# Kernel tuning notes

Hardware: AMD Instinct MI355X
Metric: run time of the kernel (lower is better)

The kernel has to match this reference:

```python
import jax, jax.numpy as jnp
import numpy as np

B, T, C, H = 4, 2048, 1024, 16
D = C // H  # head_dim = 64

def setup_inputs() -> dict:
    key = jax.random.key(0)
    k1, k2, k3 = jax.random.split(key, 3)
    x = jax.random.normal(k1, (B, T, C), dtype=jnp.float32)
    Wqkv = jax.random.normal(k2, (C, 3 * C), dtype=jnp.float32) * (C ** -0.5)
    Wout = jax.random.normal(k3, (C, C), dtype=jnp.float32) * (C ** -0.5)
    return {"x": x, "Wqkv": Wqkv, "Wout": Wout}

def reference(x, Wqkv, Wout):
    b, t, c = x.shape
    scale = D ** -0.5
    qkv = x @ Wqkv  # [B,T,3C]
    q, k, v = jnp.split(qkv, 3, axis=-1)
    # [B,H,T,D]
    q = q.reshape(b, t, H, D).transpose(0, 2, 1, 3)
    k = k.reshape(b, t, H, D).transpose(0, 2, 1, 3)
    v = v.reshape(b, t, H, D).transpose(0, 2, 1, 3)
    scores = jnp.einsum('bhqd,bhkd->bhqk', q, k) * scale
    causal = jnp.tril(jnp.ones((t, t), dtype=bool))
    scores = jnp.where(causal, scores, -jnp.inf)
    attn = jax.nn.softmax(scores, axis=-1)
    out = jnp.einsum('bhqk,bhkd->bhqd', attn, v)
    out = out.transpose(0, 2, 1, 3).reshape(b, t, c)
    return out @ Wout
```

## Files before the change

### kernel.cpp

```cpp
#include <hip/hip_runtime.h>
#include <hip/hip_bf16.h>

#define DEV __device__ __forceinline__

typedef __attribute__((ext_vector_type(4))) float f32x4;
typedef __attribute__((ext_vector_type(8))) __bf16 bf16x8;
typedef __attribute__((ext_vector_type(8))) unsigned short u16x8;
typedef __attribute__((ext_vector_type(4))) unsigned short u16x4;

DEV unsigned short f2b(float x) {
  unsigned int u = __builtin_bit_cast(unsigned int, x);
  unsigned int r = (u + 0x7fffu + ((u >> 16) & 1u)) >> 16;
  return (unsigned short)r;
}

DEV unsigned int cvtpk(float a, float b) {
  unsigned int r;
  asm("v_cvt_pk_bf16_f32 %0, %1, %2" : "=v"(r) : "v"(a), "v"(b));
  return r;
}

DEV f32x4 mfma16(u16x8 a, u16x8 b, f32x4 c) {
  return __builtin_amdgcn_mfma_f32_16x16x32_bf16(
      __builtin_bit_cast(bf16x8, a), __builtin_bit_cast(bf16x8, b), c, 0, 0, 0);
}

DEV void async16(const unsigned short* g, unsigned short* l) {
  __builtin_amdgcn_global_load_lds(
      (const __attribute__((address_space(1))) void*)g,
      (__attribute__((address_space(3))) void*)l, 16, 0, 0);
}


__global__ void k_convert(const float* __restrict__ in, unsigned short* __restrict__ out, int n8) {
  int i = blockIdx.x * 256 + threadIdx.x;
  if (i >= n8) return;
  const float4* p = (const float4*)in + (size_t)i * 2;
  float4 a = p[0], b = p[1];
  u16x8 v;
  v[0] = f2b(a.x); v[1] = f2b(a.y); v[2] = f2b(a.z); v[3] = f2b(a.w);
  v[4] = f2b(b.x); v[5] = f2b(b.y); v[6] = f2b(b.z); v[7] = f2b(b.w);
  *((u16x8*)out + i) = v;
}

__global__ void k_transpose(const float* __restrict__ in, unsigned short* __restrict__ out,
                            int R, int Cc) {
  __shared__ float tile[32][33];
  int bx = blockIdx.x * 32, by = blockIdx.y * 32;
  int tx = threadIdx.x, ty = threadIdx.y;
#pragma unroll
  for (int i = 0; i < 32; i += 8)
    tile[ty + i][tx] = in[(size_t)(by + ty + i) * Cc + bx + tx];
  __syncthreads();
#pragma unroll
  for (int i = 0; i < 32; i += 8)
    out[(size_t)(bx + ty + i) * R + by + tx] = f2b(tile[tx][ty + i]);
}


template <typename OutT>
__global__ __launch_bounds__(256, 2)
void k_gemm_bt(const unsigned short* __restrict__ A, const unsigned short* __restrict__ Bt,
               OutT* __restrict__ C, int M, int N, int K, int ldc) {
  __shared__ __align__(16) unsigned short As[128 * 32];
  __shared__ __align__(16) unsigned short Bs[128 * 32];
  const int tid = threadIdx.x;
  const int w = tid >> 6, l = tid & 63;
  const int wr = w >> 1, wc = w & 1;
  const int lo = l & 15, hi = l >> 4;
  const int m0 = blockIdx.y * 128, n0 = blockIdx.x * 128;
  const int srow = l >> 2;
  const int scol = (l & 3) * 8;
  const size_t a_base = (size_t)(m0 + 2 * w * 16 + srow) * K + scol;
  const size_t b_base = (size_t)(n0 + 2 * w * 16 + srow) * K + scol;

  f32x4 acc[4][4] = {};

  for (int kt = 0; kt < K; kt += 32) {
    async16(A + a_base + kt, &As[(2 * w) * 512]);
    async16(A + a_base + kt + (size_t)16 * K, &As[(2 * w + 1) * 512]);
    async16(Bt + b_base + kt, &Bs[(2 * w) * 512]);
    async16(Bt + b_base + kt + (size_t)16 * K, &Bs[(2 * w + 1) * 512]);
    __syncthreads();
    u16x8 af[4], bfv[4];
#pragma unroll
    for (int mi = 0; mi < 4; ++mi)
      af[mi] = *(const u16x8*)&As[(wr * 64 + mi * 16 + lo) * 32 + hi * 8];
#pragma unroll
    for (int ni = 0; ni < 4; ++ni)
      bfv[ni] = *(const u16x8*)&Bs[(wc * 64 + ni * 16 + lo) * 32 + hi * 8];
#pragma unroll
    for (int mi = 0; mi < 4; ++mi)
#pragma unroll
      for (int ni = 0; ni < 4; ++ni)
        acc[mi][ni] = mfma16(af[mi], bfv[ni], acc[mi][ni]);
    __syncthreads();
  }
#pragma unroll
  for (int mi = 0; mi < 4; ++mi) {
#pragma unroll
    for (int ni = 0; ni < 4; ++ni) {
      int col = n0 + wc * 64 + ni * 16 + lo;
#pragma unroll
      for (int r = 0; r < 4; ++r) {
        int row = m0 + wr * 64 + mi * 16 + hi * 4 + r;
        float v = acc[mi][ni][r];
        if constexpr (sizeof(OutT) == 4)
          C[(size_t)row * ldc + col] = v;
        else
          C[(size_t)row * ldc + col] = f2b(v);
      }
    }
  }
}


__global__ void k_repack_qk(const unsigned short* __restrict__ qkv,
                            unsigned short* __restrict__ q, unsigned short* __restrict__ k) {
  int idx = blockIdx.x * 256 + threadIdx.x;
  int sel = idx >> 20;
  int rem = idx & ((1 << 20) - 1);
  int m = rem >> 7;
  int ch = rem & 127;
  int h = ch >> 3, d0 = (ch & 7) * 8;
  u16x8 v = *(const u16x8*)&qkv[(size_t)m * 3072 + sel * 1024 + h * 64 + d0];
  int b = m >> 11, t = m & 2047;
  unsigned short* dst = (sel == 0 ? q : k);
  *(u16x8*)&dst[(((size_t)(b * 16 + h)) * 2048 + t) * 64 + d0] = v;
}


__global__ void k_transpose_v(const unsigned short* __restrict__ qkv,
                              unsigned short* __restrict__ vt) {
  __shared__ __align__(16) unsigned short tile[64][68];
  int bh = blockIdx.x >> 5, tt = blockIdx.x & 31;
  int b = bh >> 4, h = bh & 15;
  int t0 = tt * 64;
  int tid = threadIdx.x;
  int rr = tid >> 4, cc = (tid & 15) * 4;
#pragma unroll
  for (int i = 0; i < 4; ++i) {
    int row = rr + i * 16;
    u16x4 v = *(const u16x4*)&qkv[(size_t)(b * 2048 + t0 + row) * 3072 + 2048 + h * 64 + cc];
    *(u16x4*)&tile[row][cc] = v;
  }
  __syncthreads();
#pragma unroll
  for (int i = 0; i < 4; ++i) {
    int d = rr + i * 16;
    u16x4 v;
#pragma unroll
    for (int j = 0; j < 4; ++j) v[j] = tile[cc + j][d];
    *(u16x4*)&vt[((size_t)bh * 64 + d) * 2048 + t0 + cc] = v;
  }
}


DEV void attn_strip(const unsigned short* __restrict__ Q,
                    const unsigned short* __restrict__ Kp,
                    const unsigned short* __restrict__ Vp,
                    unsigned short* __restrict__ AO,
                    int bh, int q0, int lo, int g) {
  const size_t base = (size_t)bh * 2048 * 64;
  const unsigned short* Kb = Kp + base;
  const unsigned short* Vb = Vp + base;

  u16x8 qf[2][2];
#pragma unroll
  for (int qh = 0; qh < 2; ++qh)
#pragma unroll
    for (int dh = 0; dh < 2; ++dh)
      qf[qh][dh] = *(const u16x8*)&Q[base + (size_t)(q0 + qh * 16 + lo) * 64 + dh * 32 + g * 8];

  f32x4 o[2][4] = {};
  float m[2] = {-INFINITY, -INFINITY};
  float lsum[2] = {0.f, 0.f};

  const int nb = q0 / 32 + 1;
  u16x8 kA[2][2], kN[2][2];
#pragma unroll
  for (int kvh = 0; kvh < 2; ++kvh)
#pragma unroll
    for (int dh = 0; dh < 2; ++dh)
      kA[kvh][dh] = *(const u16x8*)&Kb[(size_t)(kvh * 16 + lo) * 64 + dh * 32 + g * 8];

  for (int blk = 0; blk < nb; ++blk) {
    const int kv0 = blk * 32;
    if (blk + 1 < nb) {
      const int kn = kv0 + 32;
#pragma unroll
      for (int kvh = 0; kvh < 2; ++kvh)
#pragma unroll
        for (int dh = 0; dh < 2; ++dh)
          kN[kvh][dh] = *(const u16x8*)&Kb[(size_t)(kn + kvh * 16 + lo) * 64 + dh * 32 + g * 8];
    }
    u16x8 vf[4];
#pragma unroll
    for (int n = 0; n < 4; ++n)
      vf[n] = *(const u16x8*)&Vb[(size_t)(n * 16 + lo) * 2048 + kv0 + g * 8];

    f32x4 sT[2][2];
#pragma unroll
    for (int qh = 0; qh < 2; ++qh)
#pragma unroll
      for (int kvh = 0; kvh < 2; ++kvh) {
        f32x4 z = {};
        z = mfma16(kA[kvh][0], qf[qh][0], z);
        z = mfma16(kA[kvh][1], qf[qh][1], z);
        sT[qh][kvh] = z;
      }

    const bool lastblk = (blk == nb - 1);
#pragma unroll
    for (int qh = 0; qh < 2; ++qh) {
      float s[8];
#pragma unroll
      for (int kvh = 0; kvh < 2; ++kvh)
#pragma unroll
        for (int r = 0; r < 4; ++r) {
          float v = sT[qh][kvh][r] * 0.125f;
          s[kvh * 4 + r] = v;
        }
      if (lastblk) {
        const int qi = qh * 16 + lo;
#pragma unroll
        for (int kvh = 0; kvh < 2; ++kvh)
#pragma unroll
          for (int r = 0; r < 4; ++r)
            if (kvh * 16 + 4 * g + r > qi) s[kvh * 4 + r] = -INFINITY;
      }
      float mx = fmaxf(fmaxf(fmaxf(s[0], s[1]), fmaxf(s[2], s[3])),
                       fmaxf(fmaxf(s[4], s[5]), fmaxf(s[6], s[7])));
      mx = fmaxf(mx, __shfl_xor(mx, 16));
      mx = fmaxf(mx, __shfl_xor(mx, 32));
      float corr = 1.0f;
      if (!__all(mx <= m[qh] + 8.0f)) {
        float mn = fmaxf(m[qh], mx);
        corr = __expf(m[qh] - mn);
        m[qh] = mn;
#pragma unroll
        for (int n = 0; n < 4; ++n)
#pragma unroll
          for (int r = 0; r < 4; ++r) o[qh][n][r] *= corr;
      }
      float pe[8];
#pragma unroll
      for (int i = 0; i < 8; ++i) pe[i] = __expf(s[i] - m[qh]);
      float rs = (pe[0] + pe[1]) + (pe[2] + pe[3]) + (pe[4] + pe[5]) + (pe[6] + pe[7]);
      rs += __shfl_xor(rs, 16);
      rs += __shfl_xor(rs, 32);
      lsum[qh] = lsum[qh] * corr + rs;

      unsigned dw0 = cvtpk(pe[0], pe[1]);
      unsigned dw1 = cvtpk(pe[2], pe[3]);
      unsigned dw2 = cvtpk(pe[4], pe[5]);
      unsigned dw3 = cvtpk(pe[6], pe[7]);
      const int srcA = lo + ((g & 1) << 5);
      const int srcB = srcA + 16;
      unsigned a0 = (unsigned)__shfl((int)dw0, srcA);
      unsigned a2 = (unsigned)__shfl((int)dw2, srcA);
      unsigned b0 = (unsigned)__shfl((int)dw1, srcA);
      unsigned b2 = (unsigned)__shfl((int)dw3, srcA);
      unsigned c0 = (unsigned)__shfl((int)dw0, srcB);
      unsigned c2 = (unsigned)__shfl((int)dw2, srcB);
      unsigned d0 = (unsigned)__shfl((int)dw1, srcB);
      unsigned d2 = (unsigned)__shfl((int)dw3, srcB);
      const bool hiK = (g >= 2);
      unsigned tw[4];
      tw[0] = hiK ? a2 : a0;
      tw[1] = hiK ? b2 : b0;
      tw[2] = hiK ? c2 : c0;
      tw[3] = hiK ? d2 : d0;
      u16x8 pB;
#pragma unroll
      for (int i = 0; i < 4; ++i) {
        pB[2 * i] = (unsigned short)(tw[i] & 0xffffu);
        pB[2 * i + 1] = (unsigned short)(tw[i] >> 16);
      }
#pragma unroll
      for (int n = 0; n < 4; ++n) o[qh][n] = mfma16(vf[n], pB, o[qh][n]);
    }

    if (blk + 1 < nb) {
#pragma unroll
      for (int kvh = 0; kvh < 2; ++kvh)
#pragma unroll
        for (int dh = 0; dh < 2; ++dh) kA[kvh][dh] = kN[kvh][dh];
    }
  }

  const int b = bh >> 4, h = bh & 15;
#pragma unroll
  for (int qh = 0; qh < 2; ++qh) {
    const float inv = 1.0f / lsum[qh];
    const int t = q0 + qh * 16 + lo;
    const size_t row = (size_t)(b * 2048 + t);
#pragma unroll
    for (int n = 0; n < 4; ++n) {
      u16x4 pk;
#pragma unroll
      for (int r = 0; r < 4; ++r) pk[r] = f2b(o[qh][n][r] * inv);
      *(u16x4*)&AO[row * 1024 + h * 64 + n * 16 + 4 * g] = pk;
    }
  }
}

__global__ __launch_bounds__(256, 2)
void k_attn(const unsigned short* __restrict__ Q, const unsigned short* __restrict__ K,
            const unsigned short* __restrict__ V, unsigned short* __restrict__ AO) {
  const int tid = threadIdx.x, w = tid >> 6, l = tid & 63;
  const int lo = l & 15, g = l >> 4;
  const int bh = blockIdx.y;
  const int p = blockIdx.x * 4 + w;
  attn_strip(Q, K, V, AO, bh, p * 32, lo, g);
  attn_strip(Q, K, V, AO, bh, (63 - p) * 32, lo, g);
}


extern "C" void kernel_launch(void* const* d_in, const int* in_sizes, int n_in,
                              void* d_out, int out_size, void* d_ws, size_t ws_size,
                              hipStream_t stream) {
  (void)in_sizes; (void)n_in; (void)out_size;
  const float* x    = (const float*)d_in[0];
  const float* Wqkv = (const float*)d_in[1];
  const float* Wout = (const float*)d_in[2];
  float* out = (float*)d_out;

  const size_t OFF_XB  = 0;
  const size_t OFF_WQT = 16777216;
  const size_t OFF_WOT = 23068672;
  const size_t OFF_Q   = 25165824;
  const size_t OFF_K   = 41943040;
  const size_t OFF_VT  = 58720256;
  const size_t OFF_QKV = 75497472;
  const size_t NEED    = 125829120;
  if (ws_size < NEED) return;

  char* ws = (char*)d_ws;
  unsigned short* xb  = (unsigned short*)(ws + OFF_XB);
  unsigned short* wqT = (unsigned short*)(ws + OFF_WQT);
  unsigned short* woT = (unsigned short*)(ws + OFF_WOT);
  unsigned short* q   = (unsigned short*)(ws + OFF_Q);
  unsigned short* kk  = (unsigned short*)(ws + OFF_K);
  unsigned short* vt  = (unsigned short*)(ws + OFF_VT);
  unsigned short* qkv = (unsigned short*)(ws + OFF_QKV);
  unsigned short* ao  = qkv;

  k_convert<<<4096, 256, 0, stream>>>(x, xb, 1048576);
  dim3 tb(32, 8);
  k_transpose<<<dim3(96, 32), tb, 0, stream>>>(Wqkv, wqT, 1024, 3072);
  k_transpose<<<dim3(32, 32), tb, 0, stream>>>(Wout, woT, 1024, 1024);
  k_gemm_bt<unsigned short><<<dim3(24, 64), 256, 0, stream>>>(xb, wqT, qkv, 8192, 3072, 1024, 3072);
  k_repack_qk<<<8192, 256, 0, stream>>>(qkv, q, kk);
  k_transpose_v<<<2048, 256, 0, stream>>>(qkv, vt);
  k_attn<<<dim3(8, 64), 256, 0, stream>>>(q, kk, vt, ao);
  k_gemm_bt<float><<<dim3(8, 64), 256, 0, stream>>>(ao, woT, out, 8192, 1024, 1024, 1024);
}
```

Baseline: 246.6 us.

## Pre-permute V^T layout to drop P shuffles; shrink attention blocks to two waves

The V transpose kernel now writes V^T with a permuted token order, so the bf16-packed softmax probabilities can feed the PV MFMA directly. This removes the eight cross-lane shuffles and selects per row-half in the attention inner loop. Separately, the attention launch uses 128-thread blocks, each pairing one early and one late causal strip, with a swizzled block-to-(batch,head) mapping and launch bounds raised to 4 blocks per CU. The cost is reliance on the permuted V layout matching the MFMA operand layout exactly, plus changed load balance and occupancy.

```diff
diff --git a/kernel.cpp b/kernel.cpp
--- a/kernel.cpp
+++ b/kernel.cpp
@@ -145,13 +145,16 @@
     *(u16x4*)&tile[row][cc] = v;
   }
   __syncthreads();
+  const int c32 = cc & 31;
+  const int sbase = (c32 < 16) ? (2 * c32) : (2 * (c32 - 16) + 4);
+  const int pos = t0 + (cc >> 5) * 32 + sbase;
 #pragma unroll
   for (int i = 0; i < 4; ++i) {
     int d = rr + i * 16;
     u16x4 v;
 #pragma unroll
     for (int j = 0; j < 4; ++j) v[j] = tile[cc + j][d];
-    *(u16x4*)&vt[((size_t)bh * 64 + d) * 2048 + t0 + cc] = v;
+    *(u16x4*)&vt[((size_t)bh * 64 + d) * 2048 + pos] = v;
   }
 }
 
@@ -217,10 +220,8 @@
 #pragma unroll
       for (int kvh = 0; kvh < 2; ++kvh)
 #pragma unroll
-        for (int r = 0; r < 4; ++r) {
-          float v = sT[qh][kvh][r] * 0.125f;
-          s[kvh * 4 + r] = v;
-        }
+        for (int r = 0; r < 4; ++r)
+          s[kvh * 4 + r] = sT[qh][kvh][r] * 0.125f;
       if (lastblk) {
         const int qi = qh * 16 + lo;
 #pragma unroll
@@ -246,31 +247,16 @@
       float pe[8];
 #pragma unroll
       for (int i = 0; i < 8; ++i) pe[i] = __expf(s[i] - m[qh]);
-      float rs = (pe[0] + pe[1]) + (pe[2] + pe[3]) + (pe[4] + pe[5]) + (pe[6] + pe[7]);
+      float rs = ((pe[0] + pe[1]) + (pe[2] + pe[3])) + ((pe[4] + pe[5]) + (pe[6] + pe[7]));
       rs += __shfl_xor(rs, 16);
       rs += __shfl_xor(rs, 32);
       lsum[qh] = lsum[qh] * corr + rs;
 
-      unsigned dw0 = cvtpk(pe[0], pe[1]);
-      unsigned dw1 = cvtpk(pe[2], pe[3]);
-      unsigned dw2 = cvtpk(pe[4], pe[5]);
-      unsigned dw3 = cvtpk(pe[6], pe[7]);
-      const int srcA = lo + ((g & 1) << 5);
-      const int srcB = srcA + 16;
-      unsigned a0 = (unsigned)__shfl((int)dw0, srcA);
-      unsigned a2 = (unsigned)__shfl((int)dw2, srcA);
-      unsigned b0 = (unsigned)__shfl((int)dw1, srcA);
-      unsigned b2 = (unsigned)__shfl((int)dw3, srcA);
-      unsigned c0 = (unsigned)__shfl((int)dw0, srcB);
-      unsigned c2 = (unsigned)__shfl((int)dw2, srcB);
-      unsigned d0 = (unsigned)__shfl((int)dw1, srcB);
-      unsigned d2 = (unsigned)__shfl((int)dw3, srcB);
-      const bool hiK = (g >= 2);
       unsigned tw[4];
-      tw[0] = hiK ? a2 : a0;
-      tw[1] = hiK ? b2 : b0;
-      tw[2] = hiK ? c2 : c0;
-      tw[3] = hiK ? d2 : d0;
+      tw[0] = cvtpk(pe[0], pe[1]);
+      tw[1] = cvtpk(pe[2], pe[3]);
+      tw[2] = cvtpk(pe[4], pe[5]);
+      tw[3] = cvtpk(pe[6], pe[7]);
       u16x8 pB;
 #pragma unroll
       for (int i = 0; i < 4; ++i) {
@@ -305,15 +291,16 @@
   }
 }
 
-__global__ __launch_bounds__(256, 2)
+__global__ __launch_bounds__(128, 4)
 void k_attn(const unsigned short* __restrict__ Q, const unsigned short* __restrict__ K,
             const unsigned short* __restrict__ V, unsigned short* __restrict__ AO) {
   const int tid = threadIdx.x, w = tid >> 6, l = tid & 63;
   const int lo = l & 15, g = l >> 4;
-  const int bh = blockIdx.y;
-  const int p = blockIdx.x * 4 + w;
-  attn_strip(Q, K, V, AO, bh, p * 32, lo, g);
-  attn_strip(Q, K, V, AO, bh, (63 - p) * 32, lo, g);
+  const int i = blockIdx.x;
+  const int bh = (i & 7) * 8 + (i >> 8);
+  const int p = (i >> 3) & 31;
+  const int strip = w ? (63 - p) : p;
+  attn_strip(Q, K, V, AO, bh, strip * 32, lo, g);
 }
 
 
@@ -353,6 +340,6 @@
   k_gemm_bt<unsigned short><<<dim3(24, 64), 256, 0, stream>>>(xb, wqT, qkv, 8192, 3072, 1024, 3072);
   k_repack_qk<<<8192, 256, 0, stream>>>(qkv, q, kk);
   k_transpose_v<<<2048, 256, 0, stream>>>(qkv, vt);
-  k_attn<<<dim3(8, 64), 256, 0, stream>>>(q, kk, vt, ao);
+  k_attn<<<2048, 128, 0, stream>>>(q, kk, vt, ao);
   k_gemm_bt<float><<<dim3(8, 64), 256, 0, stream>>>(ao, woT, out, 8192, 1024, 1024, 1024);
 }
```

Result: slower. 293.5 us (+19.0%).
